# Kernel tuning notes

Hardware: AMD Instinct MI355X
Metric: run time of the kernel (lower is better)

The kernel has to match this reference:

```python
import jax, jax.numpy as jnp
import numpy as np

B, C, H, W, K, NCLASS = 8, 512, 96, 96, 32, 19
EPS = 1e-5


def setup_inputs() -> dict:
    key = jax.random.key(0)
    ks = jax.random.split(key, 10)
    return {
        "x": jax.random.normal(ks[0], (B, C, H, W), dtype=jnp.float32),
        "conv_w": jax.random.normal(ks[1], (C, C), dtype=jnp.float32) * (1.0 / np.sqrt(C)),
        "bn2_w": jax.random.uniform(ks[2], (C,), dtype=jnp.float32, minval=0.5, maxval=1.5),
        "bn2_b": jax.random.normal(ks[3], (C,), dtype=jnp.float32) * 0.1,
        "bn2_mean": jnp.zeros((C,), jnp.float32),
        "bn2_var": jnp.ones((C,), jnp.float32),
        "codewords": jax.random.normal(ks[4], (K, C), dtype=jnp.float32) * (1.0 / np.sqrt(C)),
        "scale": jax.random.uniform(ks[5], (K,), dtype=jnp.float32, minval=-1.0, maxval=0.0),
        "bn1_w": jax.random.uniform(ks[6], (K,), dtype=jnp.float32, minval=0.5, maxval=1.5),
        "bn1_b": jax.random.normal(ks[7], (K,), dtype=jnp.float32) * 0.1,
        "bn1_mean": jnp.zeros((K,), jnp.float32),
        "bn1_var": jnp.ones((K,), jnp.float32),
        "fc_w": jax.random.normal(ks[8], (C, C), dtype=jnp.float32) * (1.0 / np.sqrt(C)),
        "fc_b": jnp.zeros((C,), jnp.float32),
        "se_w": jax.random.normal(ks[9], (NCLASS, C), dtype=jnp.float32) * (1.0 / np.sqrt(C)),
        "se_b": jnp.zeros((NCLASS,), jnp.float32),
    }


def reference(x, conv_w, bn2_w, bn2_b, bn2_mean, bn2_var,
              codewords, scale, bn1_w, bn1_b, bn1_mean, bn1_var,
              fc_w, fc_b, se_w, se_b):
    # 1x1 conv (no bias) + BN2d (inference) + ReLU
    h = jnp.einsum('oc,bchw->bohw', conv_w, x)
    s2 = bn2_w / jnp.sqrt(bn2_var + EPS)
    h = jax.nn.relu(h * s2[None, :, None, None]
                    + (bn2_b - bn2_mean * s2)[None, :, None, None])

    # Encoding: soft assignment over K codewords
    X = h.reshape(B, C, H * W).transpose(0, 2, 1)       # (B, N, C)
    x2 = jnp.sum(X * X, axis=-1)                        # (B, N)
    c2 = jnp.sum(codewords * codewords, axis=-1)        # (K,)
    xc = jnp.einsum('bnd,kd->bnk', X, codewords)        # (B, N, K)
    sl = scale[None, None, :] * (x2[:, :, None] - 2.0 * xc + c2[None, None, :])
    A = jax.nn.softmax(sl, axis=-1)                     # (B, N, K)
    # E[b,k,d] = sum_n A[b,n,k] * (X[b,n,d] - codewords[k,d])
    E = (jnp.einsum('bnk,bnd->bkd', A, X)
         - jnp.sum(A, axis=1)[:, :, None] * codewords[None, :, :])  # (B, K, C)

    # BN1d over the K channel dim (inference) + ReLU + mean over K
    s1 = bn1_w / jnp.sqrt(bn1_var + EPS)
    E = jax.nn.relu(E * s1[None, :, None] + (bn1_b - bn1_mean * s1)[None, :, None])
    en = jnp.mean(E, axis=1)                            # (B, C)

    # SE-style gate
    gamma = jax.nn.sigmoid(en @ fc_w.T + fc_b)          # (B, C)
    out = jax.nn.relu(x + x * gamma[:, :, None, None])  # (B, C, H, W)
    se = en @ se_w.T + se_b                             # (B, NCLASS)
    return (out, se)
```

## Files before the change

kernel.cpp:

```cpp
#include <hip/hip_runtime.h>
#include <math.h>

#define EPSV 1e-5f

typedef __attribute__((ext_vector_type(8))) short short8;
typedef __attribute__((ext_vector_type(4))) float f32x4;

namespace {
constexpr int NB=8, C=512, NPIX=9216, K=32, NCLS=19;

constexpr size_t o_WB    = 0;
constexpr size_t o_CWB   = 131072;
constexpr size_t o_A2    = 139264;
constexpr size_t o_B2    = 139776;
constexpr size_t o_C2    = 140288;
constexpr size_t o_X2    = 140320;
constexpr size_t o_EW    = 214048;
constexpr size_t o_ACNT  = 345120;
constexpr size_t o_EN    = 345376;
constexpr size_t o_GAMMA = 349472;
constexpr size_t o_XT    = 353568;
constexpr size_t o_EPART = 19227936;
constexpr size_t WS_NEED = o_EPART*4 + (size_t)1152*16384*2;

constexpr int NPARTS_B = 144;
constexpr int CONV_LDS = (512*64 + 64*64)*2 + 64*4;
constexpr int ENC_LDS  = 36864*2 + 2304*2 + 64*4;
}

__device__ __forceinline__ ushort f2bf(float f){
  unsigned u = __float_as_uint(f);
  return (ushort)((u + 0x7FFFu + ((u>>16)&1u)) >> 16);
}
__device__ __forceinline__ float bf2f(ushort h){
  return __uint_as_float(((unsigned)h)<<16);
}

__global__ __launch_bounds__(256) void k_prep(
    const float* __restrict__ convw, ushort* __restrict__ Wb,
    const float* __restrict__ cw,    ushort* __restrict__ cwb,
    const float* __restrict__ bn2w, const float* __restrict__ bn2b,
    const float* __restrict__ bn2m, const float* __restrict__ bn2v,
    float* __restrict__ pa, float* __restrict__ pb, float* __restrict__ c2g)
{
  const int bid = blockIdx.x, t = threadIdx.x;
  if (bid < 136){
    const float* src = (bid < 128) ? convw : cw;
    ushort* dst      = (bid < 128) ? Wb    : cwb;
    const int base   = (bid < 128) ? bid   : (bid - 128);
    int i = (base*256 + t)*8;
    float4 a = *(const float4*)(src+i), b = *(const float4*)(src+i+4);
    uint4 o;
    o.x = f2bf(a.x) | ((unsigned)f2bf(a.y)<<16);
    o.y = f2bf(a.z) | ((unsigned)f2bf(a.w)<<16);
    o.z = f2bf(b.x) | ((unsigned)f2bf(b.y)<<16);
    o.w = f2bf(b.z) | ((unsigned)f2bf(b.w)<<16);
    *(uint4*)(dst+i) = o;
  } else {
    for (int o = t; o < C; o += 256){
      float s = bn2w[o] * rsqrtf(bn2v[o] + EPSV);
      pa[o] = s;
      pb[o] = bn2b[o] - bn2m[o] * s;
    }
    int kk = t>>3, part = t&7;
    float s = 0.f;
    for (int c = part*64; c < part*64 + 64; c += 4){
      float4 w = *(const float4*)(cw + kk*512 + c);
      s += w.x*w.x + w.y*w.y + w.z*w.z + w.w*w.w;
    }
    s += __shfl_xor(s, 1);
    s += __shfl_xor(s, 2);
    s += __shfl_xor(s, 4);
    if (part == 0) c2g[kk] = s;
  }
}

__global__ __launch_bounds__(256) void k_T(const float* __restrict__ x,
                                           ushort* __restrict__ xT){
  __shared__ float xs[64*68];
  const int bid = blockIdx.x;
  const int ct = bid & 7;
  const int nt = bid >> 3;
  const int b = nt / 144, ntl = nt % 144;
  const int c0 = ct*64, n0 = ntl*64;
  const int t = threadIdx.x;
  const float* src = x + ((size_t)b*C + c0)*NPIX + n0;
#pragma unroll
  for (int p = 0; p < 4; ++p){
    const int cr = p*16 + (t>>4);
    const int nc = (t&15)*4;
    *(float4*)(xs + cr*68 + nc) = *(const float4*)(src + (size_t)cr*NPIX + nc);
  }
  __syncthreads();
  const int nr = t>>2, ck = (t&3)*16;
  uint pk[8];
#pragma unroll
  for (int j = 0; j < 8; ++j){
    float f0 = xs[(ck + 2*j  )*68 + nr];
    float f1 = xs[(ck + 2*j+1)*68 + nr];
    pk[j] = (uint)f2bf(f0) | ((uint)f2bf(f1)<<16);
  }
  ushort* dst = xT + ((size_t)(b*NPIX + n0 + nr))*512 + c0 + ck;
  *(uint4*)(dst)   = make_uint4(pk[0],pk[1],pk[2],pk[3]);
  *(uint4*)(dst+8) = make_uint4(pk[4],pk[5],pk[6],pk[7]);
}

__global__ __launch_bounds__(256,2) void k_conv(
  const ushort* __restrict__ Wb, ushort* __restrict__ xT,
  const float* __restrict__ pA2, const float* __restrict__ pB2,
  float* __restrict__ x2g)
{
  extern __shared__ char smem[];
  ushort* As  = (ushort*)smem;
  ushort* Bs  = As + 512*64;
  float*  x2s = (float*)(Bs + 64*64);
  const int t = threadIdx.x;
  const int n0 = blockIdx.x * 64;
  const int wave = t>>6, lane = t&63;
  const int lg = lane>>4, l15 = lane&15;

  if (t < 64) x2s[t] = 0.f;

  f32x4 acc[8][4];
#pragma unroll
  for (int mi = 0; mi < 8; ++mi)
#pragma unroll
    for (int nj = 0; nj < 4; ++nj) acc[mi][nj] = (f32x4){0.f,0.f,0.f,0.f};

  const int srow = t>>3, sq = t&7;
  for (int s = 0; s < 8; ++s) {
    const int c0 = s*64;
    __syncthreads();
#pragma unroll
    for (int p = 0; p < 16; ++p) {
      const int r = p*32 + srow;
      uint4 v = *(const uint4*)(Wb + r*512 + c0 + sq*8);
      *(uint4*)(As + r*64 + (((sq ^ (r&7))&7)<<3)) = v;
    }
#pragma unroll
    for (int p = 0; p < 2; ++p) {
      const int r = p*32 + srow;
      uint4 v = *(const uint4*)(xT + (size_t)(n0+r)*512 + c0 + sq*8);
      *(uint4*)(Bs + r*64 + (((sq ^ (r&7))&7)<<3)) = v;
    }
    __syncthreads();
#pragma unroll
    for (int kk = 0; kk < 2; ++kk) {
      short8 af[8], bfv[4];
#pragma unroll
      for (int mi = 0; mi < 8; ++mi) {
        const int r = wave*128 + mi*16 + l15;
        af[mi] = *(const short8*)(As + r*64 + ((((kk*4+lg) ^ (r&7))&7)<<3));
      }
#pragma unroll
      for (int nj = 0; nj < 4; ++nj) {
        const int r = nj*16 + l15;
        bfv[nj] = *(const short8*)(Bs + r*64 + ((((kk*4+lg) ^ (r&7))&7)<<3));
      }
#pragma unroll
      for (int mi = 0; mi < 8; ++mi)
#pragma unroll
        for (int nj = 0; nj < 4; ++nj)
          acc[mi][nj] = __builtin_amdgcn_mfma_f32_16x16x32_bf16(af[mi], bfv[nj], acc[mi][nj], 0,0,0);
    }
  }

  float x2p[4] = {0.f,0.f,0.f,0.f};
#pragma unroll
  for (int mi = 0; mi < 8; ++mi) {
    const int ob = wave*128 + mi*16 + lg*4;
    const float4 sa = *(const float4*)(pA2 + ob);
    const float4 sb = *(const float4*)(pB2 + ob);
#pragma unroll
    for (int nj = 0; nj < 4; ++nj) {
      const int n = n0 + nj*16 + l15;
      f32x4 a = acc[mi][nj];
      float h0 = fmaxf(fmaf(a[0], sa.x, sb.x), 0.f);
      float h1 = fmaxf(fmaf(a[1], sa.y, sb.y), 0.f);
      float h2 = fmaxf(fmaf(a[2], sa.z, sb.z), 0.f);
      float h3 = fmaxf(fmaf(a[3], sa.w, sb.w), 0.f);
      x2p[nj] += h0*h0 + h1*h1 + h2*h2 + h3*h3;
      uint2 pk;
      pk.x = f2bf(h0) | ((unsigned)f2bf(h1)<<16);
      pk.y = f2bf(h2) | ((unsigned)f2bf(h3)<<16);
      *(uint2*)(xT + (size_t)n*512 + ob) = pk;
    }
  }
#pragma unroll
  for (int nj = 0; nj < 4; ++nj) {
    float v = x2p[nj];
    v += __shfl_xor(v, 16);
    v += __shfl_xor(v, 32);
    if (lg == 0) atomicAdd(&x2s[nj*16 + l15], v);
  }
  __syncthreads();
  if (t < 64) x2g[n0 + t] = x2s[t];
}

__global__ __launch_bounds__(256,2) void k_enc2(
  const ushort* __restrict__ hT, const float* __restrict__ x2g,
  const ushort* __restrict__ cwb, const float* __restrict__ scale,
  const float* __restrict__ c2g, ushort* __restrict__ Epart,
  float* __restrict__ EwAtomic, float* __restrict__ Acnt, int useAtomic)
{
  extern __shared__ ushort sm16[];
  ushort* hbuf = sm16;
  ushort* Pl   = sm16 + 36864;
  float*  x2s  = (float*)(sm16 + 36864 + 2304);

  const int t = threadIdx.x, bid = blockIdx.x;
  const int wave = t>>6, lane = t&63, lg = lane>>4, l15 = lane&15;
  const int b = bid / NPARTS_B;
  const size_t n0 = (size_t)bid*64;

  float sc[2][4], cv[2][4];
#pragma unroll
  for (int f=0; f<2; ++f)
#pragma unroll
    for (int i=0; i<4; ++i){
      int k = f*16 + lg*4 + i;
      sc[f][i] = scale[k];
      cv[f][i] = c2g[k];
    }

  f32x4 Eacc[2][8];
#pragma unroll
  for (int f=0; f<2; ++f)
#pragma unroll
    for (int nf=0; nf<8; ++nf) Eacc[f][nf] = (f32x4){0.f,0.f,0.f,0.f};
  float acs[2][4] = {{0.f,0.f,0.f,0.f},{0.f,0.f,0.f,0.f}};

  {
    const int px = t>>2, cq = t&3;
    const ushort* src = hT + (n0+px)*512 + cq*128;
    ushort* dst = hbuf + px*520 + cq*128;
#pragma unroll
    for (int i=0; i<16; ++i)
      *(uint4*)(dst + i*8) = *(const uint4*)(src + i*8);
  }
  if (t < 64) x2s[t] = x2g[n0 + t];
  __syncthreads();

  f32x4 xacc[2];
  xacc[0] = (f32x4){0.f,0.f,0.f,0.f};
  xacc[1] = (f32x4){0.f,0.f,0.f,0.f};
  {
    const ushort* hrow  = hbuf + (wave*16 + l15)*520 + lg*8;
    const ushort* arow0 = cwb + (l15)*512 + lg*8;
    const ushort* arow1 = cwb + (16 + l15)*512 + lg*8;
#pragma unroll
    for (int s = 0; s < 16; ++s){
      short8 bfr = *(const short8*)(hrow  + s*32);
      short8 a0  = *(const short8*)(arow0 + s*32);
      short8 a1  = *(const short8*)(arow1 + s*32);
      xacc[0] = __builtin_amdgcn_mfma_f32_16x16x32_bf16(a0, bfr, xacc[0], 0,0,0);
      xacc[1] = __builtin_amdgcn_mfma_f32_16x16x32_bf16(a1, bfr, xacc[1], 0,0,0);
    }
  }
  const float x2v = x2s[wave*16 + l15];
  float sl[2][4];
  float mx = -1e30f;
#pragma unroll
  for (int f=0; f<2; ++f)
#pragma unroll
    for (int i=0; i<4; ++i){
      sl[f][i] = sc[f][i]*(x2v - 2.f*xacc[f][i] + cv[f][i]);
      mx = fmaxf(mx, sl[f][i]);
    }
  mx = fmaxf(mx, __shfl_xor(mx, 16));
  mx = fmaxf(mx, __shfl_xor(mx, 32));
  float pv[2][4];
  float ssum = 0.f;
#pragma unroll
  for (int f=0; f<2; ++f)
#pragma unroll
    for (int i=0; i<4; ++i){
      pv[f][i] = __expf(sl[f][i] - mx);
      ssum += pv[f][i];
    }
  ssum += __shfl_xor(ssum, 16);
  ssum += __shfl_xor(ssum, 32);
  const float inv = 1.f/ssum;
#pragma unroll
  for (int f=0; f<2; ++f)
#pragma unroll
    for (int i=0; i<4; ++i){
      float p = pv[f][i]*inv;
      ushort pb = f2bf(p);
      acs[f][i] += bf2f(pb);
      Pl[(f*16 + lg*4 + i)*72 + wave*16 + l15] = pb;
    }
  uint4 treg[16];
  {
    const ushort* src = hbuf + lane*520 + wave*128;
#pragma unroll
    for (int i=0; i<16; ++i) treg[i] = *(const uint4*)(src + i*8);
  }
  __syncthreads();
  {
    ushort* dstT = hbuf + (size_t)(wave*128)*72 + lane;
#pragma unroll
    for (int i=0; i<16; ++i){
      uint4 v = treg[i];
#pragma unroll
      for (int w2=0; w2<4; ++w2){
        unsigned word = (&v.x)[w2];
        dstT[(i*8 + w2*2    )*72] = (ushort)(word & 0xFFFFu);
        dstT[(i*8 + w2*2 + 1)*72] = (ushort)(word >> 16);
      }
    }
  }
  __syncthreads();
  short8 pa[2][2];
#pragma unroll
  for (int f=0; f<2; ++f)
#pragma unroll
    for (int ks=0; ks<2; ++ks)
      pa[f][ks] = *(const short8*)(Pl + (f*16 + l15)*72 + ks*32 + lg*8);
#pragma unroll
  for (int nf=0; nf<8; ++nf){
    const ushort* brow = hbuf + (size_t)(wave*128 + nf*16 + l15)*72 + lg*8;
    short8 b0 = *(const short8*)(brow);
    short8 b1 = *(const short8*)(brow + 32);
    Eacc[0][nf] = __builtin_amdgcn_mfma_f32_16x16x32_bf16(pa[0][0], b0, Eacc[0][nf], 0,0,0);
    Eacc[0][nf] = __builtin_amdgcn_mfma_f32_16x16x32_bf16(pa[0][1], b1, Eacc[0][nf], 0,0,0);
    Eacc[1][nf] = __builtin_amdgcn_mfma_f32_16x16x32_bf16(pa[1][0], b0, Eacc[1][nf], 0,0,0);
    Eacc[1][nf] = __builtin_amdgcn_mfma_f32_16x16x32_bf16(pa[1][1], b1, Eacc[1][nf], 0,0,0);
  }

  if (!useAtomic){
    ushort* pbase = Epart + (size_t)bid*16384;
#pragma unroll
    for (int f=0; f<2; ++f)
#pragma unroll
      for (int nf=0; nf<8; ++nf){
        const int c = wave*128 + nf*16 + l15;
        f32x4 a = Eacc[f][nf];
        uint2 pk;
        pk.x = f2bf(a[0]) | ((unsigned)f2bf(a[1])<<16);
        pk.y = f2bf(a[2]) | ((unsigned)f2bf(a[3])<<16);
        *(uint2*)(pbase + (size_t)c*32 + f*16 + lg*4) = pk;
      }
  } else {
    float* pbase = EwAtomic + (size_t)b*16384;
#pragma unroll
    for (int f=0; f<2; ++f)
#pragma unroll
      for (int nf=0; nf<8; ++nf){
        const int c = wave*128 + nf*16 + l15;
        float* p = pbase + (size_t)c*32 + f*16 + lg*4;
        atomicAdd(p+0, Eacc[f][nf][0]);
        atomicAdd(p+1, Eacc[f][nf][1]);
        atomicAdd(p+2, Eacc[f][nf][2]);
        atomicAdd(p+3, Eacc[f][nf][3]);
      }
  }
#pragma unroll
  for (int f=0; f<2; ++f)
#pragma unroll
    for (int i=0; i<4; ++i){
      float v = acs[f][i];
      v += __shfl_xor(v, 1);
      v += __shfl_xor(v, 2);
      v += __shfl_xor(v, 4);
      v += __shfl_xor(v, 8);
      if (l15 == 0) atomicAdd(&Acnt[b*32 + f*16 + lg*4 + i], v);
    }
}

__global__ __launch_bounds__(256) void k_en2(
    const ushort* __restrict__ Epart, const float* __restrict__ EwAtomic,
    const float* __restrict__ Acnt, const float* __restrict__ cw,
    const float* __restrict__ bn1w, const float* __restrict__ bn1b,
    const float* __restrict__ bn1m, const float* __restrict__ bn1v,
    float* __restrict__ en, int useAtomic)
{
  const int b = blockIdx.x >> 6;
  const int cchunk = blockIdx.x & 63;
  const int t = threadIdx.x;
  const int c_local = t >> 5, k = t & 31;
  const int c = cchunk*8 + c_local;

  float acc = 0.f;
  if (!useAtomic){
    const ushort* base = Epart + (size_t)b*NPARTS_B*16384 + cchunk*256 + t;
    for (int g = 0; g < NPARTS_B; ++g)
      acc += bf2f(base[(size_t)g*16384]);
  } else {
    acc = EwAtomic[(size_t)b*16384 + (size_t)c*32 + k];
  }
  float s1 = bn1w[k]*rsqrtf(bn1v[k]+EPSV);
  float t1 = bn1b[k] - bn1m[k]*s1;
  float e = acc - Acnt[b*32 + k]*cw[(size_t)k*512 + c];
  float v = fmaxf(fmaf(e, s1, t1), 0.f);
  v += __shfl_xor(v, 1);
  v += __shfl_xor(v, 2);
  v += __shfl_xor(v, 4);
  v += __shfl_xor(v, 8);
  v += __shfl_xor(v, 16);
  if (k == 0) en[(size_t)b*512 + c] = v*(1.f/32.f);
}

__global__ __launch_bounds__(512) void k_gate(
    const float* __restrict__ en, const float* __restrict__ fcw,
    const float* __restrict__ fcb, const float* __restrict__ sew,
    const float* __restrict__ seb, float* __restrict__ gamma,
    float* __restrict__ se_out)
{
    __shared__ float es[C];
    const int b = blockIdx.x;
    es[threadIdx.x] = en[(size_t)b * C + threadIdx.x];
    __syncthreads();
    {
        const int c = threadIdx.x;
        float z = fcb[c];
        const float* wr = fcw + (size_t)c * C;
        for (int i = 0; i < C; i += 4) {
            const float4 w = *(const float4*)(wr + i);
            z += w.x * es[i] + w.y * es[i + 1] + w.z * es[i + 2] + w.w * es[i + 3];
        }
        gamma[(size_t)b * C + c] = 1.f / (1.f + expf(-z));
    }
    if (threadIdx.x < NCLS * 8) {
        const int j = threadIdx.x >> 3, lane = threadIdx.x & 7;
        float p = 0.f;
        const float* swr = sew + (size_t)j * C;
        for (int i = lane * 64; i < lane * 64 + 64; i += 4) {
            const float4 w = *(const float4*)(swr + i);
            p += w.x * es[i] + w.y * es[i + 1] + w.z * es[i + 2] + w.w * es[i + 3];
        }
        p += __shfl_xor(p, 1);
        p += __shfl_xor(p, 2);
        p += __shfl_xor(p, 4);
        if (lane == 0) se_out[b * NCLS + j] = p + seb[j];
    }
}

__global__ __launch_bounds__(256) void k_out(
    const float* __restrict__ x, const float* __restrict__ gamma,
    float* __restrict__ out)
{
    const int total4 = NB * C * NPIX / 4;
    for (int i = blockIdx.x * blockDim.x + threadIdx.x; i < total4;
         i += gridDim.x * blockDim.x) {
        const int flat = i * 4;
        const int bc = flat / NPIX;
        const float gsc = 1.f + gamma[bc];
        float4 v = *(const float4*)(x + flat);
        v.x = fmaxf(v.x * gsc, 0.f);
        v.y = fmaxf(v.y * gsc, 0.f);
        v.z = fmaxf(v.z * gsc, 0.f);
        v.w = fmaxf(v.w * gsc, 0.f);
        *(float4*)(out + flat) = v;
    }
}

extern "C" void kernel_launch(void* const* d_in, const int* in_sizes, int n_in,
                              void* d_out, int out_size, void* d_ws, size_t ws_size,
                              hipStream_t stream)
{
    const float* x     = (const float*)d_in[0];
    const float* convw = (const float*)d_in[1];
    const float* bn2w  = (const float*)d_in[2];
    const float* bn2b  = (const float*)d_in[3];
    const float* bn2m  = (const float*)d_in[4];
    const float* bn2v  = (const float*)d_in[5];
    const float* cw    = (const float*)d_in[6];
    const float* scale = (const float*)d_in[7];
    const float* bn1w  = (const float*)d_in[8];
    const float* bn1b  = (const float*)d_in[9];
    const float* bn1m  = (const float*)d_in[10];
    const float* bn1v  = (const float*)d_in[11];
    const float* fcw   = (const float*)d_in[12];
    const float* fcb   = (const float*)d_in[13];
    const float* sew   = (const float*)d_in[14];
    const float* seb   = (const float*)d_in[15];

    float* ws = (float*)d_ws;
    float* out = (float*)d_out;
    float* se_out = out + (size_t)NB * C * NPIX;

    ushort* Wb    = (ushort*)(ws + o_WB);
    ushort* cwb   = (ushort*)(ws + o_CWB);
    ushort* xT    = (ushort*)(ws + o_XT);
    ushort* Epart = (ushort*)(ws + o_EPART);

    const bool use_part = ws_size >= WS_NEED;
    const int useAtomic = use_part ? 0 : 1;

    (void)hipFuncSetAttribute((const void*)k_conv,
                              hipFuncAttributeMaxDynamicSharedMemorySize, CONV_LDS);
    (void)hipFuncSetAttribute((const void*)k_enc2,
                              hipFuncAttributeMaxDynamicSharedMemorySize, ENC_LDS);

    hipMemsetAsync(ws + o_EW, 0, (size_t)(NB*C*K + 256) * sizeof(float), stream);

    k_prep<<<137, 256, 0, stream>>>(convw, Wb, cw, cwb,
                                    bn2w, bn2b, bn2m, bn2v,
                                    ws + o_A2, ws + o_B2, ws + o_C2);
    k_T<<<9216, 256, 0, stream>>>(x, xT);
    k_conv<<<1152, 256, CONV_LDS, stream>>>(Wb, xT, ws + o_A2, ws + o_B2, ws + o_X2);
    k_enc2<<<1152, 256, ENC_LDS, stream>>>(xT, ws + o_X2, cwb, scale, ws + o_C2,
                                           Epart, ws + o_EW, ws + o_ACNT, useAtomic);
    k_en2<<<512, 256, 0, stream>>>(Epart, ws + o_EW, ws + o_ACNT, cw,
                                   bn1w, bn1b, bn1m, bn1v, ws + o_EN, useAtomic);
    k_gate<<<8, 512, 0, stream>>>(ws + o_EN, fcw, fcb, sew, seb,
                                  ws + o_GAMMA, se_out);
    k_out<<<2048, 256, 0, stream>>>(x, ws + o_GAMMA, out);
}
```

Measured before the change: 362.9 us.

## Fuse conv+BN+ReLU with encoding kernel, keeping activations in LDS

Merges the 1x1-conv kernel and the encoding kernel into one kernel. The bf16 activation tile for 64 pixels now stays in shared memory and feeds the codeword distance and aggregation MFMAs directly, instead of being written back to global memory and reloaded. This drops a full global write and read of the activations (about 75MB) plus one launch. It also reuses the conv LDS region for the activation tile, adds a barrier, and computes x2 from the rounded bf16 values. LDS per block stays near the previous conv size, so occupancy should be unchanged.

```diff
diff --git a/kernel.cpp b/kernel.cpp
--- a/kernel.cpp
+++ b/kernel.cpp
@@ -24,8 +24,7 @@
 constexpr size_t WS_NEED = o_EPART*4 + (size_t)1152*16384*2;
 
 constexpr int NPARTS_B = 144;
-constexpr int CONV_LDS = (512*64 + 64*64)*2 + 64*4;
-constexpr int ENC_LDS  = 36864*2 + 2304*2 + 64*4;
+constexpr int FUSED_LDS = 78592;
 }
 
 __device__ __forceinline__ ushort f2bf(float f){
@@ -105,19 +104,26 @@
   *(uint4*)(dst+8) = make_uint4(pk[4],pk[5],pk[6],pk[7]);
 }
 
-__global__ __launch_bounds__(256,2) void k_conv(
-  const ushort* __restrict__ Wb, ushort* __restrict__ xT,
+__global__ __launch_bounds__(256,2) void k_fused(
+  const ushort* __restrict__ Wb, const ushort* __restrict__ xT,
+  const ushort* __restrict__ cwb,
   const float* __restrict__ pA2, const float* __restrict__ pB2,
-  float* __restrict__ x2g)
+  const float* __restrict__ scale, const float* __restrict__ c2g,
+  ushort* __restrict__ Epart, float* __restrict__ EwAtomic,
+  float* __restrict__ Acnt, int useAtomic)
 {
   extern __shared__ char smem[];
   ushort* As  = (ushort*)smem;
   ushort* Bs  = As + 512*64;
-  float*  x2s = (float*)(Bs + 64*64);
-  const int t = threadIdx.x;
-  const int n0 = blockIdx.x * 64;
+  ushort* hs  = (ushort*)smem;
+  ushort* Pl  = (ushort*)(smem + 73728);
+  float*  x2s = (float*)(smem + 78336);
+
+  const int t = threadIdx.x, bid = blockIdx.x;
   const int wave = t>>6, lane = t&63;
   const int lg = lane>>4, l15 = lane&15;
+  const int b = bid / NPARTS_B;
+  const size_t n0 = (size_t)bid * 64;
 
   if (t < 64) x2s[t] = 0.f;
 
@@ -140,7 +146,7 @@
 #pragma unroll
     for (int p = 0; p < 2; ++p) {
       const int r = p*32 + srow;
-      uint4 v = *(const uint4*)(xT + (size_t)(n0+r)*512 + c0 + sq*8);
+      uint4 v = *(const uint4*)(xT + (n0+r)*512 + c0 + sq*8);
       *(uint4*)(Bs + r*64 + (((sq ^ (r&7))&7)<<3)) = v;
     }
     __syncthreads();
@@ -164,6 +170,7 @@
           acc[mi][nj] = __builtin_amdgcn_mfma_f32_16x16x32_bf16(af[mi], bfv[nj], acc[mi][nj], 0,0,0);
     }
   }
+  __syncthreads();
 
   float x2p[4] = {0.f,0.f,0.f,0.f};
 #pragma unroll
@@ -173,17 +180,19 @@
     const float4 sb = *(const float4*)(pB2 + ob);
 #pragma unroll
     for (int nj = 0; nj < 4; ++nj) {
-      const int n = n0 + nj*16 + l15;
+      const int px = nj*16 + l15;
       f32x4 a = acc[mi][nj];
       float h0 = fmaxf(fmaf(a[0], sa.x, sb.x), 0.f);
       float h1 = fmaxf(fmaf(a[1], sa.y, sb.y), 0.f);
       float h2 = fmaxf(fmaf(a[2], sa.z, sb.z), 0.f);
       float h3 = fmaxf(fmaf(a[3], sa.w, sb.w), 0.f);
-      x2p[nj] += h0*h0 + h1*h1 + h2*h2 + h3*h3;
       uint2 pk;
       pk.x = f2bf(h0) | ((unsigned)f2bf(h1)<<16);
       pk.y = f2bf(h2) | ((unsigned)f2bf(h3)<<16);
-      *(uint2*)(xT + (size_t)n*512 + ob) = pk;
+      *(uint2*)(hs + px*520 + ob) = pk;
+      h0 = bf2f((ushort)(pk.x & 0xFFFFu)); h1 = bf2f((ushort)(pk.x >> 16));
+      h2 = bf2f((ushort)(pk.y & 0xFFFFu)); h3 = bf2f((ushort)(pk.y >> 16));
+      x2p[nj] += h0*h0 + h1*h1 + h2*h2 + h3*h3;
     }
   }
 #pragma unroll
@@ -194,24 +203,6 @@
     if (lg == 0) atomicAdd(&x2s[nj*16 + l15], v);
   }
   __syncthreads();
-  if (t < 64) x2g[n0 + t] = x2s[t];
-}
-
-__global__ __launch_bounds__(256,2) void k_enc2(
-  const ushort* __restrict__ hT, const float* __restrict__ x2g,
-  const ushort* __restrict__ cwb, const float* __restrict__ scale,
-  const float* __restrict__ c2g, ushort* __restrict__ Epart,
-  float* __restrict__ EwAtomic, float* __restrict__ Acnt, int useAtomic)
-{
-  extern __shared__ ushort sm16[];
-  ushort* hbuf = sm16;
-  ushort* Pl   = sm16 + 36864;
-  float*  x2s  = (float*)(sm16 + 36864 + 2304);
-
-  const int t = threadIdx.x, bid = blockIdx.x;
-  const int wave = t>>6, lane = t&63, lg = lane>>4, l15 = lane&15;
-  const int b = bid / NPARTS_B;
-  const size_t n0 = (size_t)bid*64;
 
   float sc[2][4], cv[2][4];
 #pragma unroll
@@ -223,29 +214,11 @@
       cv[f][i] = c2g[k];
     }
 
-  f32x4 Eacc[2][8];
-#pragma unroll
-  for (int f=0; f<2; ++f)
-#pragma unroll
-    for (int nf=0; nf<8; ++nf) Eacc[f][nf] = (f32x4){0.f,0.f,0.f,0.f};
-  float acs[2][4] = {{0.f,0.f,0.f,0.f},{0.f,0.f,0.f,0.f}};
-
-  {
-    const int px = t>>2, cq = t&3;
-    const ushort* src = hT + (n0+px)*512 + cq*128;
-    ushort* dst = hbuf + px*520 + cq*128;
-#pragma unroll
-    for (int i=0; i<16; ++i)
-      *(uint4*)(dst + i*8) = *(const uint4*)(src + i*8);
-  }
-  if (t < 64) x2s[t] = x2g[n0 + t];
-  __syncthreads();
-
   f32x4 xacc[2];
   xacc[0] = (f32x4){0.f,0.f,0.f,0.f};
   xacc[1] = (f32x4){0.f,0.f,0.f,0.f};
   {
-    const ushort* hrow  = hbuf + (wave*16 + l15)*520 + lg*8;
+    const ushort* hrow  = hs + (wave*16 + l15)*520 + lg*8;
     const ushort* arow0 = cwb + (l15)*512 + lg*8;
     const ushort* arow1 = cwb + (16 + l15)*512 + lg*8;
 #pragma unroll
@@ -281,24 +254,25 @@
   ssum += __shfl_xor(ssum, 16);
   ssum += __shfl_xor(ssum, 32);
   const float inv = 1.f/ssum;
+  float acs[2][4];
 #pragma unroll
   for (int f=0; f<2; ++f)
 #pragma unroll
     for (int i=0; i<4; ++i){
       float p = pv[f][i]*inv;
       ushort pb = f2bf(p);
-      acs[f][i] += bf2f(pb);
+      acs[f][i] = bf2f(pb);
       Pl[(f*16 + lg*4 + i)*72 + wave*16 + l15] = pb;
     }
   uint4 treg[16];
   {
-    const ushort* src = hbuf + lane*520 + wave*128;
+    const ushort* src = hs + lane*520 + wave*128;
 #pragma unroll
     for (int i=0; i<16; ++i) treg[i] = *(const uint4*)(src + i*8);
   }
   __syncthreads();
   {
-    ushort* dstT = hbuf + (size_t)(wave*128)*72 + lane;
+    ushort* dstT = hs + (size_t)(wave*128)*72 + lane;
 #pragma unroll
     for (int i=0; i<16; ++i){
       uint4 v = treg[i];
@@ -311,6 +285,11 @@
     }
   }
   __syncthreads();
+  f32x4 Eacc[2][8];
+#pragma unroll
+  for (int f=0; f<2; ++f)
+#pragma unroll
+    for (int nf=0; nf<8; ++nf) Eacc[f][nf] = (f32x4){0.f,0.f,0.f,0.f};
   short8 pa[2][2];
 #pragma unroll
   for (int f=0; f<2; ++f)
@@ -319,7 +298,7 @@
       pa[f][ks] = *(const short8*)(Pl + (f*16 + l15)*72 + ks*32 + lg*8);
 #pragma unroll
   for (int nf=0; nf<8; ++nf){
-    const ushort* brow = hbuf + (size_t)(wave*128 + nf*16 + l15)*72 + lg*8;
+    const ushort* brow = hs + (size_t)(wave*128 + nf*16 + l15)*72 + lg*8;
     short8 b0 = *(const short8*)(brow);
     short8 b1 = *(const short8*)(brow + 32);
     Eacc[0][nf] = __builtin_amdgcn_mfma_f32_16x16x32_bf16(pa[0][0], b0, Eacc[0][nf], 0,0,0);
@@ -488,10 +467,8 @@
     const bool use_part = ws_size >= WS_NEED;
     const int useAtomic = use_part ? 0 : 1;
 
-    (void)hipFuncSetAttribute((const void*)k_conv,
-                              hipFuncAttributeMaxDynamicSharedMemorySize, CONV_LDS);
-    (void)hipFuncSetAttribute((const void*)k_enc2,
-                              hipFuncAttributeMaxDynamicSharedMemorySize, ENC_LDS);
+    (void)hipFuncSetAttribute((const void*)k_fused,
+                              hipFuncAttributeMaxDynamicSharedMemorySize, FUSED_LDS);
 
     hipMemsetAsync(ws + o_EW, 0, (size_t)(NB*C*K + 256) * sizeof(float), stream);
 
@@ -499,9 +476,10 @@
                                     bn2w, bn2b, bn2m, bn2v,
                                     ws + o_A2, ws + o_B2, ws + o_C2);
     k_T<<<9216, 256, 0, stream>>>(x, xT);
-    k_conv<<<1152, 256, CONV_LDS, stream>>>(Wb, xT, ws + o_A2, ws + o_B2, ws + o_X2);
-    k_enc2<<<1152, 256, ENC_LDS, stream>>>(xT, ws + o_X2, cwb, scale, ws + o_C2,
-                                           Epart, ws + o_EW, ws + o_ACNT, useAtomic);
+    k_fused<<<1152, 256, FUSED_LDS, stream>>>(Wb, xT, cwb,
+                                              ws + o_A2, ws + o_B2,
+                                              scale, ws + o_C2,
+                                              Epart, ws + o_EW, ws + o_ACNT, useAtomic);
     k_en2<<<512, 256, 0, stream>>>(Epart, ws + o_EW, ws + o_ACNT, cw,
                                    bn1w, bn1b, bn1m, bn1v, ws + o_EN, useAtomic);
     k_gate<<<8, 512, 0, stream>>>(ws + o_EN, fcw, fcb, sew, seb,
```

Measured after the change: 329.9 us. 1.1x faster.
